# Kernel optimization log

Hardware: AMD Instinct MI355X
Metric: run time of the kernel (lower is better)

Reference implementation:

```python
import jax, jax.numpy as jnp
import numpy as np

WS = (4, 4, 4)  # window shape (wd, wh, ww)
EPS = 1e-5


def _layernorm(x, g, b):
    mu = jnp.mean(x, axis=-1, keepdims=True)
    var = jnp.mean(jnp.square(x - mu), axis=-1, keepdims=True)
    return (x - mu) * jax.lax.rsqrt(var + EPS) * g + b


def _partition(x, ws):
    # x: [B, D, H, W, C] -> [num_windows, wd*wh*ww, C]
    B, D, H, W, C = x.shape
    x = x.reshape(B, D // ws[0], ws[0], H // ws[1], ws[1], W // ws[2], ws[2], C)
    x = jnp.transpose(x, (0, 1, 3, 5, 2, 4, 6, 7))
    return x.reshape(-1, ws[0] * ws[1] * ws[2], C)


def _merge(win, shape, ws):
    B, D, H, W, C = shape
    x = win.reshape(B, D // ws[0], H // ws[1], W // ws[2], ws[0], ws[1], ws[2], C)
    x = jnp.transpose(x, (0, 1, 4, 2, 5, 3, 6, 7))
    return x.reshape(B, D, H, W, C)


def setup_inputs() -> dict:
    key = jax.random.key(0)
    ks = jax.random.split(key, 8)
    B, D, H, W, C = 2, 32, 64, 64, 96
    nh, kd = 4, 24
    s = 0.02
    return {
        "x": jax.random.normal(ks[0], (B, D, H, W, C), jnp.float32),
        "ln1_g": jnp.ones((C,), jnp.float32),
        "ln1_b": jnp.zeros((C,), jnp.float32),
        "wq": jax.random.normal(ks[1], (C, nh, kd), jnp.float32) * s,
        "bq": jnp.zeros((nh, kd), jnp.float32),
        "wk": jax.random.normal(ks[2], (C, nh, kd), jnp.float32) * s,
        "bk": jnp.zeros((nh, kd), jnp.float32),
        "wv": jax.random.normal(ks[3], (C, nh, kd), jnp.float32) * s,
        "bv": jnp.zeros((nh, kd), jnp.float32),
        "wo": jax.random.normal(ks[4], (nh, kd, C), jnp.float32) * s,
        "bo": jnp.zeros((C,), jnp.float32),
        "ln2_g": jnp.ones((C,), jnp.float32),
        "ln2_b": jnp.zeros((C,), jnp.float32),
        "w1": jax.random.normal(ks[5], (C, 4 * C), jnp.float32) * s,
        "b1": jnp.zeros((4 * C,), jnp.float32),
        "w2": jax.random.normal(ks[6], (4 * C, C), jnp.float32) * s,
        "b2": jnp.zeros((C,), jnp.float32),
    }


def reference(x, ln1_g, ln1_b, wq, bq, wk, bk, wv, bv, wo, bo,
              ln2_g, ln2_b, w1, b1, w2, b2):
    shape = x.shape  # [B, D, H, W, C]; dims chosen divisible by WS -> pad is a no-op
    kd = wq.shape[-1]
    shortcut = x
    h = _layernorm(x, ln1_g, ln1_b)
    win = _partition(h, WS)  # [n, L, C], L = 64
    # Keras MultiHeadAttention (inference, dropout off)
    q = jnp.einsum("nlc,chd->nlhd", win, wq) + bq
    k = jnp.einsum("nlc,chd->nlhd", win, wk) + bk
    v = jnp.einsum("nlc,chd->nlhd", win, wv) + bv
    scores = jnp.einsum("nlhd,nmhd->nhlm", q, k) / jnp.sqrt(jnp.float32(kd))
    attn = jax.nn.softmax(scores, axis=-1)
    o = jnp.einsum("nhlm,nmhd->nlhd", attn, v)
    out = jnp.einsum("nlhd,hdc->nlc", o, wo) + bo
    x = shortcut + _merge(out, shape, WS)
    shortcut = x
    h = _layernorm(x, ln2_g, ln2_b)
    h = jax.nn.gelu(h @ w1 + b1, approximate=False)  # TF keras 'gelu' is exact
    h = h @ w2 + b2
    return shortcut + h
```

## Files before the change

### kernel.cpp

```cpp
#include <hip/hip_runtime.h>
#include <hip/hip_bf16.h>

typedef __attribute__((ext_vector_type(8))) short short8;
typedef __attribute__((ext_vector_type(4))) short short4b;
typedef __attribute__((ext_vector_type(4))) float f32x4;
typedef unsigned short ushort_t;

#define NTOK 262144

__device__ __forceinline__ ushort_t f2bf(float f){
  __hip_bfloat16 h = __float2bfloat16(f);
  return *reinterpret_cast<ushort_t*>(&h);
}
__device__ __forceinline__ float bf2f(ushort_t u){
  union { unsigned int i; float f; } v; v.i = ((unsigned int)u) << 16; return v.f;
}
__device__ __forceinline__ float fast_rcp(float x){
  float r; asm("v_rcp_f32 %0, %1" : "=v"(r) : "v"(x)); return r;
}
__device__ __forceinline__ float gelu_f(float x){
  float x2 = x * x;
  float z = x * fmaf(0.0356774081f, x2, 0.7978845608f);
  float e = __expf(2.0f * z);
  float t = 1.0f - 2.0f * fast_rcp(e + 1.0f);
  return 0.5f * x * (1.0f + t);
}
__device__ __forceinline__ void bar_lds(){
  asm volatile("s_waitcnt lgkmcnt(0)" ::: "memory");
  __builtin_amdgcn_s_barrier();
  __builtin_amdgcn_sched_barrier(0);
}
__device__ __forceinline__ void bar_cnt5(){
  asm volatile("s_waitcnt vmcnt(5) lgkmcnt(0)" ::: "memory");
  __builtin_amdgcn_s_barrier();
  __builtin_amdgcn_sched_barrier(0);
}
__device__ __forceinline__ void bar_cnt0(){
  asm volatile("s_waitcnt vmcnt(0) lgkmcnt(0)" ::: "memory");
  __builtin_amdgcn_s_barrier();
  __builtin_amdgcn_sched_barrier(0);
}
__device__ __forceinline__ void gl_lds16(const ushort_t* g, ushort_t* l){
  __builtin_amdgcn_global_load_lds(
      (const __attribute__((address_space(1))) void*)g,
      (__attribute__((address_space(3))) void*)l, 16, 0, 0);
}

template<int NT>
__device__ __forceinline__ void stage_w(const ushort_t* __restrict__ src,
                                        int src_stride, ushort_t (*dst)[104], int tid)
{
  #pragma unroll
  for (int it = 0; it < (1248 + NT - 1) / NT; ++it) {
    int u = tid + it * NT;
    if (u < 1248) {
      int row = u / 13, c16 = u % 13;
      const ushort_t* sp = src + row * src_stride + ((c16 == 12) ? 0 : c16 * 8);
      gl_lds16(sp, &dst[0][0] + (size_t)(u & ~63) * 8);
    }
  }
}

__device__ __forceinline__ void stage_wp(const ushort_t* __restrict__ src,
                                         int src_stride, ushort_t* __restrict__ dst, int tid)
{
  #pragma unroll
  for (int it = 0; it < 5; ++it) {
    int u = tid + it * 256;
    int row = u / 13, c16 = u % 13;
    const ushort_t* sp = src + row * src_stride + ((c16 >= 12) ? 0 : c16 * 8);
    gl_lds16(sp, dst + (size_t)(u & ~63) * 8);
  }
}

__global__ __launch_bounds__(256) void prep_kernel(
    const float* __restrict__ wq, const float* __restrict__ wk, const float* __restrict__ wv,
    const float* __restrict__ wo, const float* __restrict__ w1, const float* __restrict__ w2,
    const float* __restrict__ bq, const float* __restrict__ bk, const float* __restrict__ bv,
    ushort_t* __restrict__ Wqkv, ushort_t* __restrict__ Wo,
    ushort_t* __restrict__ W1, ushort_t* __restrict__ W2, float* __restrict__ biasq)
{
  const float qs = 0.20412414523193150818f;
  int i = blockIdx.x * 256 + threadIdx.x;
  if (i < 27648) {
    int j = i / 96, c = i % 96;
    int s = j / 96, rem = j % 96;
    const float* src = (s == 0) ? wq : (s == 1) ? wk : wv;
    float val = src[c * 96 + rem];
    if (s == 0) val *= qs;
    Wqkv[j * 96 + c] = f2bf(val);
  } else if (i < 36864) {
    int ii = i - 27648;
    int c = ii / 96, hd = ii % 96;
    Wo[ii] = f2bf(wo[hd * 96 + c]);
  } else if (i < 73728) {
    int ii = i - 36864;
    int j = ii / 96, c = ii % 96;
    W1[ii] = f2bf(w1[c * 384 + j]);
  } else if (i < 110592) {
    int ii = i - 73728;
    int c = ii / 384, j = ii % 384;
    W2[ii] = f2bf(w2[j * 96 + c]);
  } else if (i < 110880) {
    int j = i - 110592;
    int s = j / 96, rem = j % 96;
    const float* src = (s == 0) ? bq : (s == 1) ? bk : bv;
    float val = src[rem];
    if (s == 0) val *= qs;
    biasq[j] = val;
  }
}

__global__ __launch_bounds__(256, 2) void fat_kernel(
    const float* __restrict__ x, const float* __restrict__ g, const float* __restrict__ b,
    const ushort_t* __restrict__ Wqkv, const float* __restrict__ biasq,
    const ushort_t* __restrict__ Wo, const float* __restrict__ bo,
    ushort_t* __restrict__ x2b)
{
  __shared__ ushort_t regionA[20480];
  __shared__ ushort_t Vt[4][32][72];
  __shared__ ushort_t Ws[96][104];
  ushort_t (*hbt)[104]   = reinterpret_cast<ushort_t(*)[104]>(regionA);
  ushort_t (*QK)[216]    = reinterpret_cast<ushort_t(*)[216]>(regionA + 64 * 104);
  ushort_t (*Pb)[64][72] = reinterpret_cast<ushort_t(*)[64][72]>(regionA);
  ushort_t (*O_lds)[104] = reinterpret_cast<ushort_t(*)[104]>(regionA);

  int tid = threadIdx.x;
  int n = blockIdx.x;
  int wq_ = n & 15, hq = (n >> 4) & 15, rest = n >> 8;
  int dq = rest & 7, bb_ = rest >> 3;
  int base = bb_ * 131072 + dq * 16384 + hq * 256 + wq_ * 4;
  #define TOK(s) (base + ((s) >> 4) * 4096 + (((s) >> 2) & 3) * 64 + ((s) & 3))

  stage_w<256>(Wqkv, 96, Ws, tid);

  {
    int s = tid >> 2, qr = tid & 3;
    const float* xp = x + (size_t)TOK(s) * 96 + qr * 24;
    f32x4 v[6];
    float sm = 0.f, sq = 0.f;
    #pragma unroll
    for (int i = 0; i < 6; i++) {
      v[i] = *reinterpret_cast<const f32x4*>(xp + i * 4);
      #pragma unroll
      for (int j = 0; j < 4; j++) { sm += v[i][j]; sq += v[i][j] * v[i][j]; }
    }
    sm += __shfl_xor(sm, 1); sq += __shfl_xor(sq, 1);
    sm += __shfl_xor(sm, 2); sq += __shfl_xor(sq, 2);
    float mean = sm * (1.0f / 96.0f);
    float var  = sq * (1.0f / 96.0f) - mean * mean;
    float rstd = rsqrtf(var + 1e-5f);
    #pragma unroll
    for (int i8 = 0; i8 < 3; i8++) {
      short8 pk;
      #pragma unroll
      for (int j = 0; j < 8; j++) {
        int c = qr * 24 + i8 * 8 + j;
        pk[j] = (short)f2bf((v[(i8 * 8 + j) >> 2][(i8 * 8 + j) & 3] - mean) * rstd * g[c] + b[c]);
      }
      *reinterpret_cast<short8*>(&hbt[s][qr * 24 + i8 * 8]) = pk;
    }
  }
  __syncthreads();

  int w = tid >> 6, lane = tid & 63, g16 = lane >> 4, l15 = lane & 15;
  short8 af[3];
  #pragma unroll
  for (int ks = 0; ks < 3; ks++)
    af[ks] = *reinterpret_cast<const short8*>(&hbt[w * 16 + l15][ks * 32 + g16 * 8]);

  for (int grp = 0; grp < 3; ++grp) {
    f32x4 acc[6];
    #pragma unroll
    for (int j = 0; j < 6; j++) acc[j] = (f32x4){0.f, 0.f, 0.f, 0.f};
    #pragma unroll
    for (int j = 0; j < 6; j++)
      #pragma unroll
      for (int ks = 0; ks < 3; ks++) {
        short8 wfr = *reinterpret_cast<const short8*>(&Ws[j * 16 + l15][ks * 32 + g16 * 8]);
        acc[j] = __builtin_amdgcn_mfma_f32_16x16x32_bf16(wfr, af[ks], acc[j], 0, 0, 0);
      }
    bar_lds();
    if (grp < 2) stage_w<256>(Wqkv + (grp + 1) * 9216, 96, Ws, tid);
    else         stage_w<256>(Wo, 96, Ws, tid);
    if (grp < 2) {
      #pragma unroll
      for (int j = 0; j < 6; j++) {
        int c0 = grp * 96 + j * 16 + g16 * 4;
        f32x4 bb4 = *reinterpret_cast<const f32x4*>(&biasq[c0]);
        unsigned lo = (unsigned)f2bf(acc[j][0] + bb4[0]) | ((unsigned)f2bf(acc[j][1] + bb4[1]) << 16);
        unsigned hi = (unsigned)f2bf(acc[j][2] + bb4[2]) | ((unsigned)f2bf(acc[j][3] + bb4[3]) << 16);
        uint2 pk; pk.x = lo; pk.y = hi;
        *reinterpret_cast<uint2*>(&QK[w * 16 + l15][c0]) = pk;
      }
    } else {
      #pragma unroll
      for (int j = 0; j < 6; j++) {
        int c0 = j * 16 + g16 * 4;
        f32x4 bb4 = *reinterpret_cast<const f32x4*>(&biasq[192 + c0]);
        #pragma unroll
        for (int r = 0; r < 4; r++) {
          int vcol = c0 + r;
          int h2 = vcol / 24, d2 = vcol - h2 * 24;
          Vt[h2][d2][w * 16 + l15] = f2bf(acc[j][r] + bb4[r]);
        }
      }
    }
    __syncthreads();
  }

  int h = w;
  short8 kf[4], qf[4];
  const short8 z8 = {0, 0, 0, 0, 0, 0, 0, 0};
  #pragma unroll
  for (int i = 0; i < 4; i++) {
    qf[i] = (g16 < 3) ? *(const short8*)&QK[i * 16 + l15][h * 24 + g16 * 8]      : z8;
    kf[i] = (g16 < 3) ? *(const short8*)&QK[i * 16 + l15][96 + h * 24 + g16 * 8] : z8;
  }
  f32x4 st[4][4];
  #pragma unroll
  for (int tm = 0; tm < 4; tm++)
    #pragma unroll
    for (int tn = 0; tn < 4; tn++)
      st[tm][tn] = __builtin_amdgcn_mfma_f32_16x16x32_bf16(kf[tm], qf[tn],
                    (f32x4){0.f, 0.f, 0.f, 0.f}, 0, 0, 0);
  bar_lds();

  #pragma unroll
  for (int tn = 0; tn < 4; tn++) {
    float m = st[0][tn][0];
    #pragma unroll
    for (int tm = 0; tm < 4; tm++)
      #pragma unroll
      for (int r = 0; r < 4; r++) m = fmaxf(m, st[tm][tn][r]);
    m = fmaxf(m, __shfl_xor(m, 16));
    m = fmaxf(m, __shfl_xor(m, 32));
    float sum = 0.f;
    #pragma unroll
    for (int tm = 0; tm < 4; tm++)
      #pragma unroll
      for (int r = 0; r < 4; r++) {
        float e = __expf(st[tm][tn][r] - m);
        st[tm][tn][r] = e;
        sum += e;
      }
    sum += __shfl_xor(sum, 16);
    sum += __shfl_xor(sum, 32);
    float inv = fast_rcp(sum);
    int q = tn * 16 + l15;
    #pragma unroll
    for (int tm = 0; tm < 4; tm++) {
      unsigned lo = (unsigned)f2bf(st[tm][tn][0] * inv) | ((unsigned)f2bf(st[tm][tn][1] * inv) << 16);
      unsigned hi = (unsigned)f2bf(st[tm][tn][2] * inv) | ((unsigned)f2bf(st[tm][tn][3] * inv) << 16);
      uint2 pk; pk.x = lo; pk.y = hi;
      *(uint2*)&Pb[h][q][tm * 16 + g16 * 4] = pk;
    }
  }

  f32x4 oacc[4][2];
  #pragma unroll
  for (int qt = 0; qt < 4; qt++)
    #pragma unroll
    for (int dt = 0; dt < 2; dt++) oacc[qt][dt] = (f32x4){0.f, 0.f, 0.f, 0.f};
  #pragma unroll
  for (int ks = 0; ks < 2; ks++) {
    short8 vb[2];
    #pragma unroll
    for (int dt = 0; dt < 2; dt++)
      vb[dt] = *(const short8*)&Vt[h][dt * 16 + l15][ks * 32 + g16 * 8];
    #pragma unroll
    for (int qt = 0; qt < 4; qt++) {
      short8 pa = *(const short8*)&Pb[h][qt * 16 + l15][ks * 32 + g16 * 8];
      #pragma unroll
      for (int dt = 0; dt < 2; dt++)
        oacc[qt][dt] = __builtin_amdgcn_mfma_f32_16x16x32_bf16(pa, vb[dt], oacc[qt][dt], 0, 0, 0);
    }
  }

  __syncthreads();
  #pragma unroll
  for (int qt = 0; qt < 4; qt++)
    #pragma unroll
    for (int dt = 0; dt < 2; dt++) {
      int d = dt * 16 + l15;
      if (d < 24) {
        #pragma unroll
        for (int r = 0; r < 4; r++)
          O_lds[qt * 16 + g16 * 4 + r][h * 24 + d] = f2bf(oacc[qt][dt][r]);
      }
    }
  __syncthreads();

  f32x4 pacc[6];
  #pragma unroll
  for (int nt = 0; nt < 6; nt++) pacc[nt] = (f32x4){0.f, 0.f, 0.f, 0.f};
  #pragma unroll
  for (int ks = 0; ks < 3; ks++) {
    short8 pa = *(const short8*)&O_lds[w * 16 + l15][ks * 32 + g16 * 8];
    #pragma unroll
    for (int nt = 0; nt < 6; nt++) {
      short8 wb = *reinterpret_cast<const short8*>(&Ws[nt * 16 + l15][ks * 32 + g16 * 8]);
      pacc[nt] = __builtin_amdgcn_mfma_f32_16x16x32_bf16(pa, wb, pacc[nt], 0, 0, 0);
    }
  }
  #pragma unroll
  for (int nt = 0; nt < 6; nt++) {
    int col = nt * 16 + l15;
    float bs = bo[col];
    #pragma unroll
    for (int r = 0; r < 4; r++) {
      int s2 = w * 16 + g16 * 4 + r;
      size_t t = (size_t)TOK(s2);
      float v = pacc[nt][r] + bs + x[t * 96 + col];
      x2b[t * 96 + col] = f2bf(v);
    }
  }
  #undef TOK
}

__device__ __forceinline__ void ln_to_lds_b(const ushort_t* __restrict__ xrow_base,
    const float* __restrict__ gg, const float* __restrict__ bb,
    ushort_t (*hbt)[104], int tid)
{
  int row = tid >> 1, half = tid & 1;
  const ushort_t* xp = xrow_base + (size_t)row * 96 + half * 48;
  short8 vv[6];
  #pragma unroll
  for (int i = 0; i < 6; i++) vv[i] = *reinterpret_cast<const short8*>(xp + i * 8);
  float v[48];
  float s = 0.f, sq = 0.f;
  #pragma unroll
  for (int i = 0; i < 6; i++)
    #pragma unroll
    for (int j = 0; j < 8; j++) {
      float f = bf2f((ushort_t)vv[i][j]);
      v[i * 8 + j] = f; s += f; sq += f * f;
    }
  s  += __shfl_xor(s, 1);
  sq += __shfl_xor(sq, 1);
  float mean = s * (1.0f / 96.0f);
  float var  = sq * (1.0f / 96.0f) - mean * mean;
  float rstd = rsqrtf(var + 1e-5f);
  #pragma unroll
  for (int i8 = 0; i8 < 6; i8++) {
    short8 pk;
    #pragma unroll
    for (int j = 0; j < 8; j++) {
      int c = half * 48 + i8 * 8 + j;
      pk[j] = (short)f2bf((v[i8 * 8 + j] - mean) * rstd * gg[c] + bb[c]);
    }
    *reinterpret_cast<short8*>(&hbt[row][half * 48 + i8 * 8]) = pk;
  }
}

__global__ __launch_bounds__(256, 2) void mlp2_kernel(
    const ushort_t* __restrict__ x2b, const float* __restrict__ g, const float* __restrict__ b,
    const ushort_t* __restrict__ W1t, const float* __restrict__ b1,
    const ushort_t* __restrict__ W2t, const float* __restrict__ b2,
    float* __restrict__ out)
{
  __shared__ ushort_t smem[128][104];
  __shared__ ushort_t WsA[10240];
  __shared__ ushort_t WsB[10240];
  __shared__ float bias1[384];
  __shared__ float bias2[96];
  int tid = threadIdx.x;
  size_t r0 = (size_t)blockIdx.x * 128;

  stage_wp(W1t, 96, WsA, tid);
  stage_wp(W2t, 384, WsB, tid);
  bias1[tid] = b1[tid];
  if (tid < 128) bias1[256 + tid] = b1[256 + tid];
  if (tid < 96)  bias2[tid] = b2[tid];
  ln_to_lds_b(x2b + r0 * 96, g, b, smem, tid);

  int w = tid >> 6, lane = tid & 63, g16 = lane >> 4, l15 = lane & 15;
  short8 af[2][3];
  #pragma unroll
  for (int mi = 0; mi < 2; mi++)
    #pragma unroll
    for (int ks = 0; ks < 3; ks++)
      af[mi][ks] = *reinterpret_cast<const short8*>(&smem[w * 32 + mi * 16 + l15][ks * 32 + g16 * 8]);
  __builtin_amdgcn_sched_barrier(0);

  f32x4 oacc[6][2];
  #pragma unroll
  for (int nt = 0; nt < 6; nt++) { oacc[nt][0] = (f32x4){0.f,0.f,0.f,0.f}; oacc[nt][1] = (f32x4){0.f,0.f,0.f,0.f}; }

  for (int cc = 0; cc < 4; ++cc) {
    bar_cnt5();
    f32x4 acc[6][2];
    #pragma unroll
    for (int nt = 0; nt < 6; nt++) { acc[nt][0] = (f32x4){0.f,0.f,0.f,0.f}; acc[nt][1] = (f32x4){0.f,0.f,0.f,0.f}; }
    #pragma unroll
    for (int nt = 0; nt < 6; nt++)
      #pragma unroll
      for (int ks = 0; ks < 3; ks++) {
        short8 wfr = *reinterpret_cast<const short8*>(&WsA[(nt * 16 + l15) * 104 + ks * 32 + g16 * 8]);
        acc[nt][0] = __builtin_amdgcn_mfma_f32_16x16x32_bf16(wfr, af[0][ks], acc[nt][0], 0, 0, 0);
        acc[nt][1] = __builtin_amdgcn_mfma_f32_16x16x32_bf16(wfr, af[1][ks], acc[nt][1], 0, 0, 0);
      }
    #pragma unroll
    for (int nt = 0; nt < 6; nt++) {
      f32x4 bb4 = *reinterpret_cast<const f32x4*>(&bias1[cc * 96 + nt * 16 + g16 * 4]);
      #pragma unroll
      for (int mi = 0; mi < 2; mi++) {
        float g0 = gelu_f(acc[nt][mi][0] + bb4[0]);
        float g1 = gelu_f(acc[nt][mi][1] + bb4[1]);
        float g2 = gelu_f(acc[nt][mi][2] + bb4[2]);
        float g3 = gelu_f(acc[nt][mi][3] + bb4[3]);
        unsigned lo = (unsigned)f2bf(g0) | ((unsigned)f2bf(g1) << 16);
        unsigned hi = (unsigned)f2bf(g2) | ((unsigned)f2bf(g3) << 16);
        uint2 pk; pk.x = lo; pk.y = hi;
        *reinterpret_cast<uint2*>(&smem[w * 32 + mi * 16 + l15][nt * 16 + g16 * 4]) = pk;
      }
    }
    short8 a2[2][3];
    #pragma unroll
    for (int mi = 0; mi < 2; mi++)
      #pragma unroll
      for (int ks = 0; ks < 3; ks++)
        a2[mi][ks] = *reinterpret_cast<const short8*>(&smem[w * 32 + mi * 16 + l15][ks * 32 + g16 * 8]);
    bar_lds();
    if (cc < 3) stage_wp(W1t + (cc + 1) * 9216, 96, WsA, tid);
    if (cc < 3) bar_cnt5(); else bar_cnt0();
    #pragma unroll
    for (int nt = 0; nt < 6; nt++)
      #pragma unroll
      for (int ks = 0; ks < 3; ks++) {
        short8 wfr = *reinterpret_cast<const short8*>(&WsB[(nt * 16 + l15) * 104 + ks * 32 + g16 * 8]);
        oacc[nt][0] = __builtin_amdgcn_mfma_f32_16x16x32_bf16(wfr, a2[0][ks], oacc[nt][0], 0, 0, 0);
        oacc[nt][1] = __builtin_amdgcn_mfma_f32_16x16x32_bf16(wfr, a2[1][ks], oacc[nt][1], 0, 0, 0);
      }
    if (cc < 3) {
      bar_lds();
      stage_wp(W2t + (cc + 1) * 96, 384, WsB, tid);
    }
  }

  #pragma unroll
  for (int nt = 0; nt < 6; nt++) {
    int c0 = nt * 16 + g16 * 4;
    f32x4 bb4 = *reinterpret_cast<const f32x4*>(&bias2[c0]);
    #pragma unroll
    for (int mi = 0; mi < 2; mi++) {
      size_t row = r0 + w * 32 + mi * 16 + l15;
      short4b rr = *reinterpret_cast<const short4b*>(&x2b[row * 96 + c0]);
      f32x4 o;
      #pragma unroll
      for (int r = 0; r < 4; r++) o[r] = oacc[nt][mi][r] + bb4[r] + bf2f((ushort_t)rr[r]);
      *reinterpret_cast<f32x4*>(&out[row * 96 + c0]) = o;
    }
  }
}

extern "C" void kernel_launch(void* const* d_in, const int* in_sizes, int n_in,
                              void* d_out, int out_size, void* d_ws, size_t ws_size,
                              hipStream_t stream)
{
  (void)in_sizes; (void)n_in; (void)out_size; (void)ws_size;
  const float* x    = (const float*)d_in[0];
  const float* ln1g = (const float*)d_in[1];
  const float* ln1b = (const float*)d_in[2];
  const float* wq   = (const float*)d_in[3];
  const float* bq   = (const float*)d_in[4];
  const float* wk   = (const float*)d_in[5];
  const float* bk   = (const float*)d_in[6];
  const float* wv   = (const float*)d_in[7];
  const float* bv   = (const float*)d_in[8];
  const float* wo   = (const float*)d_in[9];
  const float* bo   = (const float*)d_in[10];
  const float* ln2g = (const float*)d_in[11];
  const float* ln2b = (const float*)d_in[12];
  const float* w1   = (const float*)d_in[13];
  const float* b1   = (const float*)d_in[14];
  const float* w2   = (const float*)d_in[15];
  const float* b2   = (const float*)d_in[16];

  char* ws = (char*)d_ws;
  ushort_t* x2b  = (ushort_t*)(ws);
  char* wsw      = ws + 50331648;
  ushort_t* Wqkv = (ushort_t*)(wsw);
  ushort_t* Wo   = (ushort_t*)(wsw + 55296);
  ushort_t* W1   = (ushort_t*)(wsw + 55296 + 18432);
  ushort_t* W2   = (ushort_t*)(wsw + 55296 + 18432 + 73728);
  float*    biasq= (float*)   (wsw + 55296 + 18432 + 73728 + 73728);

  prep_kernel<<<434, 256, 0, stream>>>(wq, wk, wv, wo, w1, w2, bq, bk, bv,
                                       Wqkv, Wo, W1, W2, biasq);
  fat_kernel<<<4096, 256, 0, stream>>>(x, ln1g, ln1b, Wqkv, biasq, Wo, bo, x2b);
  mlp2_kernel<<<NTOK / 128, 256, 0, stream>>>(x2b, ln2g, ln2b, W1, b1, W2, b2, (float*)d_out);
}
```

Before: 186.0 us.

## Use sigmoid GELU approximation, raise wave priority around MFMAs, vectorize residual store

Replaces the tanh-form GELU with the cheaper x*sigmoid(1.702x) approximation, wraps every MFMA loop in s_setprio(1)/s_setprio(0), and swaps the MFMA operand order in the output projection so each lane holds four contiguous columns. That lets the residual add use vector loads of x and bo and a packed 8-byte bf16 store instead of scalar strided accesses. The sigmoid GELU is less accurate than the exact erf GELU the reference uses and may drift past tolerance.

Measured after the change: 183.3 us. About the same (-1.5%).

```diff
diff --git a/kernel.cpp b/kernel.cpp
--- a/kernel.cpp
+++ b/kernel.cpp
@@ -19,11 +19,8 @@
   float r; asm("v_rcp_f32 %0, %1" : "=v"(r) : "v"(x)); return r;
 }
 __device__ __forceinline__ float gelu_f(float x){
-  float x2 = x * x;
-  float z = x * fmaf(0.0356774081f, x2, 0.7978845608f);
-  float e = __expf(2.0f * z);
-  float t = 1.0f - 2.0f * fast_rcp(e + 1.0f);
-  return 0.5f * x * (1.0f + t);
+  float e = __expf(-1.702f * x);
+  return x * fast_rcp(1.0f + e);
 }
 __device__ __forceinline__ void bar_lds(){
   asm volatile("s_waitcnt lgkmcnt(0)" ::: "memory");
@@ -173,6 +170,7 @@
     f32x4 acc[6];
     #pragma unroll
     for (int j = 0; j < 6; j++) acc[j] = (f32x4){0.f, 0.f, 0.f, 0.f};
+    __builtin_amdgcn_s_setprio(1);
     #pragma unroll
     for (int j = 0; j < 6; j++)
       #pragma unroll
@@ -180,6 +178,7 @@
         short8 wfr = *reinterpret_cast<const short8*>(&Ws[j * 16 + l15][ks * 32 + g16 * 8]);
         acc[j] = __builtin_amdgcn_mfma_f32_16x16x32_bf16(wfr, af[ks], acc[j], 0, 0, 0);
       }
+    __builtin_amdgcn_s_setprio(0);
     bar_lds();
     if (grp < 2) stage_w<256>(Wqkv + (grp + 1) * 9216, 96, Ws, tid);
     else         stage_w<256>(Wo, 96, Ws, tid);
@@ -218,12 +217,14 @@
     kf[i] = (g16 < 3) ? *(const short8*)&QK[i * 16 + l15][96 + h * 24 + g16 * 8] : z8;
   }
   f32x4 st[4][4];
+  __builtin_amdgcn_s_setprio(1);
   #pragma unroll
   for (int tm = 0; tm < 4; tm++)
     #pragma unroll
     for (int tn = 0; tn < 4; tn++)
       st[tm][tn] = __builtin_amdgcn_mfma_f32_16x16x32_bf16(kf[tm], qf[tn],
                     (f32x4){0.f, 0.f, 0.f, 0.f}, 0, 0, 0);
+  __builtin_amdgcn_s_setprio(0);
   bar_lds();
 
   #pragma unroll
@@ -262,6 +263,7 @@
   for (int qt = 0; qt < 4; qt++)
     #pragma unroll
     for (int dt = 0; dt < 2; dt++) oacc[qt][dt] = (f32x4){0.f, 0.f, 0.f, 0.f};
+  __builtin_amdgcn_s_setprio(1);
   #pragma unroll
   for (int ks = 0; ks < 2; ks++) {
     short8 vb[2];
@@ -276,6 +278,7 @@
         oacc[qt][dt] = __builtin_amdgcn_mfma_f32_16x16x32_bf16(pa, vb[dt], oacc[qt][dt], 0, 0, 0);
     }
   }
+  __builtin_amdgcn_s_setprio(0);
 
   __syncthreads();
   #pragma unroll
@@ -294,25 +297,32 @@
   f32x4 pacc[6];
   #pragma unroll
   for (int nt = 0; nt < 6; nt++) pacc[nt] = (f32x4){0.f, 0.f, 0.f, 0.f};
+  __builtin_amdgcn_s_setprio(1);
   #pragma unroll
   for (int ks = 0; ks < 3; ks++) {
     short8 pa = *(const short8*)&O_lds[w * 16 + l15][ks * 32 + g16 * 8];
     #pragma unroll
     for (int nt = 0; nt < 6; nt++) {
       short8 wb = *reinterpret_cast<const short8*>(&Ws[nt * 16 + l15][ks * 32 + g16 * 8]);
-      pacc[nt] = __builtin_amdgcn_mfma_f32_16x16x32_bf16(pa, wb, pacc[nt], 0, 0, 0);
-    }
-  }
-  #pragma unroll
-  for (int nt = 0; nt < 6; nt++) {
-    int col = nt * 16 + l15;
-    float bs = bo[col];
-    #pragma unroll
-    for (int r = 0; r < 4; r++) {
-      int s2 = w * 16 + g16 * 4 + r;
-      size_t t = (size_t)TOK(s2);
-      float v = pacc[nt][r] + bs + x[t * 96 + col];
-      x2b[t * 96 + col] = f2bf(v);
+      pacc[nt] = __builtin_amdgcn_mfma_f32_16x16x32_bf16(wb, pa, pacc[nt], 0, 0, 0);
+    }
+  }
+  __builtin_amdgcn_s_setprio(0);
+  {
+    size_t t = (size_t)TOK(w * 16 + l15);
+    #pragma unroll
+    for (int nt = 0; nt < 6; nt++) {
+      int c0 = nt * 16 + g16 * 4;
+      f32x4 bo4 = *reinterpret_cast<const f32x4*>(&bo[c0]);
+      f32x4 xr  = *reinterpret_cast<const f32x4*>(&x[t * 96 + c0]);
+      float v0 = pacc[nt][0] + bo4[0] + xr[0];
+      float v1 = pacc[nt][1] + bo4[1] + xr[1];
+      float v2 = pacc[nt][2] + bo4[2] + xr[2];
+      float v3 = pacc[nt][3] + bo4[3] + xr[3];
+      unsigned lo = (unsigned)f2bf(v0) | ((unsigned)f2bf(v1) << 16);
+      unsigned hi = (unsigned)f2bf(v2) | ((unsigned)f2bf(v3) << 16);
+      uint2 pk; pk.x = lo; pk.y = hi;
+      *reinterpret_cast<uint2*>(&x2b[t * 96 + c0]) = pk;
     }
   }
   #undef TOK
@@ -392,6 +402,7 @@
     f32x4 acc[6][2];
     #pragma unroll
     for (int nt = 0; nt < 6; nt++) { acc[nt][0] = (f32x4){0.f,0.f,0.f,0.f}; acc[nt][1] = (f32x4){0.f,0.f,0.f,0.f}; }
+    __builtin_amdgcn_s_setprio(1);
     #pragma unroll
     for (int nt = 0; nt < 6; nt++)
       #pragma unroll
@@ -400,6 +411,7 @@
         acc[nt][0] = __builtin_amdgcn_mfma_f32_16x16x32_bf16(wfr, af[0][ks], acc[nt][0], 0, 0, 0);
         acc[nt][1] = __builtin_amdgcn_mfma_f32_16x16x32_bf16(wfr, af[1][ks], acc[nt][1], 0, 0, 0);
       }
+    __builtin_amdgcn_s_setprio(0);
     #pragma unroll
     for (int nt = 0; nt < 6; nt++) {
       f32x4 bb4 = *reinterpret_cast<const f32x4*>(&bias1[cc * 96 + nt * 16 + g16 * 4]);
@@ -424,6 +436,7 @@
     bar_lds();
     if (cc < 3) stage_wp(W1t + (cc + 1) * 9216, 96, WsA, tid);
     if (cc < 3) bar_cnt5(); else bar_cnt0();
+    __builtin_amdgcn_s_setprio(1);
     #pragma unroll
     for (int nt = 0; nt < 6; nt++)
       #pragma unroll
@@ -432,6 +445,7 @@
         oacc[nt][0] = __builtin_amdgcn_mfma_f32_16x16x32_bf16(wfr, a2[0][ks], oacc[nt][0], 0, 0, 0);
         oacc[nt][1] = __builtin_amdgcn_mfma_f32_16x16x32_bf16(wfr, a2[1][ks], oacc[nt][1], 0, 0, 0);
       }
+    __builtin_amdgcn_s_setprio(0);
     if (cc < 3) {
       bar_lds();
       stage_wp(W2t + (cc + 1) * 96, 384, WsB, tid);
```
